# Performance work log

Hardware: AMD Instinct MI355X
Metric: run time of the kernel (lower is better)

## Reference

```python
import jax, jax.numpy as jnp
import numpy as np

B, S, E, H = 2, 2048, 1024, 16
DH = E // H


def setup_inputs() -> dict:
    key = jax.random.key(0)
    ks = jax.random.split(key, 9)
    inp = {
        "query": jax.random.normal(ks[0], (B, S, E), dtype=jnp.float32),
        "key": jax.random.normal(ks[1], (B, S, E), dtype=jnp.float32),
        "value": jax.random.normal(ks[2], (B, S, E), dtype=jnp.float32),
        # causal mask: True means "masked out" (masked_fill semantics)
        "mask": jnp.broadcast_to(
            jnp.triu(jnp.ones((S, S), dtype=bool), k=1)[None, None], (B, 1, S, S)
        ),
        # learned parameters (nn.Linear weight is [out, in]; y = x @ W.T + b)
        "Wq": jax.random.normal(ks[3], (E, E), dtype=jnp.float32) / np.sqrt(E),
        "Wk": jax.random.normal(ks[4], (E, E), dtype=jnp.float32) / np.sqrt(E),
        "Wv": jax.random.normal(ks[5], (E, E), dtype=jnp.float32) / np.sqrt(E),
        "Wo": jax.random.normal(ks[6], (E, E), dtype=jnp.float32) / np.sqrt(E),
        "bo": jax.random.normal(ks[7], (E,), dtype=jnp.float32) * 0.01,
    }
    return inp


def reference(query, key, value, mask, Wq, Wk, Wv, Wo, bo):
    # projections (no bias for q/k/v)
    Q = query @ Wq.T  # [B,S,E]
    K = key @ Wk.T
    V = value @ Wv.T
    # split heads: [B,S,E] -> [B,H,S,Dh]
    Q = Q.reshape(B, S, H, DH).transpose(0, 2, 1, 3)
    K = K.reshape(B, S, H, DH).transpose(0, 2, 1, 3)
    V = V.reshape(B, S, H, DH).transpose(0, 2, 1, 3)
    scale = 1.0 / np.sqrt(DH).astype(np.float32)
    scores = jnp.einsum("bhqd,bhkd->bhqk", Q, K) * scale  # [B,H,S,S]
    scores = jnp.where(mask, -jnp.inf, scores)
    attn = jax.nn.softmax(scores, axis=-1)
    # dropout(p=0.2) is identity in eval mode
    out = jnp.einsum("bhqk,bhkd->bhqd", attn, V)  # [B,H,S,Dh]
    out = out.transpose(0, 2, 1, 3).reshape(B, S, E)
    return out @ Wo.T + bo
```

## Files before the change

kernel.cpp:

```cpp
#include <hip/hip_runtime.h>
#include <hip/hip_bf16.h>
#include <stdint.h>

#define Bb 2
#define Ss 2048
#define Ee 1024
#define Hh 16
#define Dh 64

typedef __bf16 bf16_t;
typedef __attribute__((ext_vector_type(8))) __bf16 bf16x8;
typedef __attribute__((ext_vector_type(4))) __bf16 bf16x4;
typedef __attribute__((ext_vector_type(4))) float f32x4;

#define QSCALE_LOG2E 0.18033688011112042f

__device__ inline void gload_lds16(const void* g, void* l) {
  __builtin_amdgcn_global_load_lds((__attribute__((address_space(1))) void*)g,
                                   (__attribute__((address_space(3))) void*)l,
                                   16, 0, 0);
}

__device__ inline void wg_barrier() {
  asm volatile("s_barrier" ::: "memory");
}

__device__ __forceinline__ int p_addr(int q, int kv) {
  return q * 256 + ((((kv >> 3) ^ q) & 15) << 4) + (kv & 7) * 2;
}

struct Cvt7 {
  const float* s[7];
  bf16_t* d[7];
  int n8[7];
};

__global__ __launch_bounds__(256) void cvt_f32_bf16(Cvt7 c) {
  int gid = blockIdx.x * 256 + threadIdx.x;
#pragma unroll
  for (int j = 0; j < 7; ++j) {
    if (gid < c.n8[j]) {
      const float* s = c.s[j] + (size_t)gid * 8;
      const f32x4 lo = *(const f32x4*)s;
      const f32x4 hi = *(const f32x4*)(s + 4);
      bf16x8 v;
      v[0] = (bf16_t)lo[0]; v[1] = (bf16_t)lo[1];
      v[2] = (bf16_t)lo[2]; v[3] = (bf16_t)lo[3];
      v[4] = (bf16_t)hi[0]; v[5] = (bf16_t)hi[1];
      v[6] = (bf16_t)hi[2]; v[7] = (bf16_t)hi[3];
      *(bf16x8*)(c.d[j] + (size_t)gid * 8) = v;
      return;
    }
    gid -= c.n8[j];
  }
}

template <int ROWS>
__device__ __forceinline__ void stage_bf16(const bf16_t* __restrict__ src,
                                           int ldk, int k0, bf16_t* lds,
                                           int wave, int lane) {
  const int srow = lane >> 3, sslot = lane & 7;
#pragma unroll
  for (int r = 0; r < ROWS / 32; ++r) {
    const int chunk = wave + r * 4;
    const int row = chunk * 8 + srow;
    const int k16 = sslot ^ (row & 7);
    gload_lds16(src + (size_t)row * ldk + k0 + k16 * 8, lds + chunk * 512);
  }
}

template <typename EPI>
__device__ __forceinline__ void gemm_128x64(const bf16_t* Arow,
                                            const bf16_t* Wrow, bf16_t* As,
                                            bf16_t* Bs, int wave, int lane,
                                            EPI epi) {
  const int lr = lane & 15, lg = lane >> 4;
  f32x4 acc[2][4] = {};

  stage_bf16<128>(Arow, Ee, 0, As, wave, lane);
  stage_bf16<64>(Wrow, Ee, 0, Bs, wave, lane);
  stage_bf16<128>(Arow, Ee, 64, As + 8192, wave, lane);
  stage_bf16<64>(Wrow, Ee, 64, Bs + 4096, wave, lane);

  for (int t = 0; t < 16; ++t) {
    const int cur = t & 1;
    if (t < 15)
      asm volatile("s_waitcnt vmcnt(6)" ::: "memory");
    else
      asm volatile("s_waitcnt vmcnt(0)" ::: "memory");
    wg_barrier();

    const char* a_base = (const char*)(As + cur * 8192);
    const char* b_base = (const char*)(Bs + cur * 4096);
#pragma unroll
    for (int kk = 0; kk < 2; ++kk) {
      bf16x8 af[2], bfr[4];
#pragma unroll
      for (int x = 0; x < 2; ++x) {
        const int arow = wave * 32 + x * 16 + lr;
        af[x] = *(const bf16x8*)(a_base + ((arow * 128 + kk * 64 + lg * 16) ^
                                           ((arow & 7) << 4)));
      }
#pragma unroll
      for (int ni = 0; ni < 4; ++ni) {
        const int brow = ni * 16 + lr;
        bfr[ni] = *(const bf16x8*)(b_base + ((brow * 128 + kk * 64 + lg * 16) ^
                                             ((brow & 7) << 4)));
      }
#pragma unroll
      for (int mi = 0; mi < 2; ++mi)
#pragma unroll
        for (int ni = 0; ni < 4; ++ni)
          acc[mi][ni] = __builtin_amdgcn_mfma_f32_16x16x32_bf16(
              af[mi], bfr[ni], acc[mi][ni], 0, 0, 0);
    }
    wg_barrier();
    if (t + 2 < 16) {
      stage_bf16<128>(Arow, Ee, (t + 2) * 64, As + cur * 8192, wave, lane);
      stage_bf16<64>(Wrow, Ee, (t + 2) * 64, Bs + cur * 4096, wave, lane);
    }
  }

#pragma unroll
  for (int mi = 0; mi < 2; ++mi)
#pragma unroll
    for (int i = 0; i < 4; ++i) {
      const int mloc = wave * 32 + mi * 16 + lg * 4 + i;
#pragma unroll
      for (int ni = 0; ni < 4; ++ni)
        epi(mloc, ni * 16 + lr, acc[mi][ni][i]);
    }
}

__global__ __launch_bounds__(256) void qkv_proj(
    const bf16_t* __restrict__ Aq, const bf16_t* __restrict__ Ak,
    const bf16_t* __restrict__ Av, const bf16_t* __restrict__ Wq,
    const bf16_t* __restrict__ Wk, const bf16_t* __restrict__ Wv,
    bf16_t* __restrict__ Cq, bf16_t* __restrict__ Ck,
    bf16_t* __restrict__ Cv) {
  __shared__ bf16_t As[2][128 * 64];
  __shared__ bf16_t Bs[2][64 * 64];
  const int z = blockIdx.z;
  const bf16_t* A = (z == 0) ? Aq : (z == 1) ? Ak : Av;
  const bf16_t* W = (z == 0) ? Wq : (z == 1) ? Wk : Wv;
  bf16_t* C = (z == 0) ? Cq : (z == 1) ? Ck : Cv;

  const int wg = blockIdx.y * 16 + blockIdx.x;
  const int virt = (wg & 7) * 64 + (wg >> 3);
  const int n0 = (virt & 15) * 64, m0 = (virt >> 4) * 128;

  const int lane = threadIdx.x & 63, wave = threadIdx.x >> 6;

  gemm_128x64(A + (size_t)m0 * Ee, W + (size_t)n0 * Ee, As[0], Bs[0], wave,
              lane, [&](int mloc, int nloc, float v) {
                const int m = m0 + mloc, n = n0 + nloc;
                if (z == 0) v *= QSCALE_LOG2E;
                const int b = m >> 11, s = m & (Ss - 1);
                const int h = n >> 6, d = n & 63;
                if (z != 2)
                  C[(((size_t)(b * Hh + h)) * Ss + s) * Dh + d] = (bf16_t)v;
                else
                  C[(((size_t)(b * Hh + h)) * Dh + d) * Ss + s] = (bf16_t)v;
              });
}

__global__ __launch_bounds__(256) void out_gemm(const bf16_t* __restrict__ A,
                                                const bf16_t* __restrict__ W,
                                                const float* __restrict__ bias,
                                                float* __restrict__ C) {
  __shared__ bf16_t As[2][128 * 64];
  __shared__ bf16_t Bs[2][64 * 64];
  const int wg = blockIdx.y * 16 + blockIdx.x;
  const int virt = (wg & 7) * 64 + (wg >> 3);
  const int n0 = (virt & 15) * 64, m0 = (virt >> 4) * 128;

  const int lane = threadIdx.x & 63, wave = threadIdx.x >> 6;

  gemm_128x64(A + (size_t)m0 * Ee, W + (size_t)n0 * Ee, As[0], Bs[0], wave,
              lane, [&](int mloc, int nloc, float v) {
                const int n = n0 + nloc;
                C[(size_t)(m0 + mloc) * Ee + n] = v + bias[n];
              });
}


__device__ __forceinline__ void attn_stage(const bf16_t* Kh, const bf16_t* Vh,
                                           int kv0, int wave, int lane,
                                           bf16_t* KsBuf, bf16_t* VsBuf) {
#pragma unroll
  for (int r = 0; r < 8; ++r) {
    const int c = wave + r * 2;
    const int krow = c * 8 + (lane >> 3);
    const int ks = (lane & 7) ^ (krow & 7);
    gload_lds16(Kh + (size_t)(kv0 + krow) * Dh + ks * 8, KsBuf + c * 512);
    const int vrow = c * 4 + (lane >> 4);
    const int vs = (lane & 15) ^ (vrow & 7);
    gload_lds16(Vh + (size_t)vrow * Ss + kv0 + vs * 8, VsBuf + c * 512);
  }
}

template <int NI, bool MASKED>
__device__ __forceinline__ void attn_tile_compute(
    int kv0, int qw, int lane, char* pb, const char* kb, const char* vb,
    const bf16x8 aq[2][2], float m_run[2], float l_run[2], f32x4 oacc[2][4]) {
  const int lr = lane & 15, lg = lane >> 4;

  f32x4 sc[2][NI];
#pragma unroll
  for (int ni = 0; ni < NI; ++ni) {
    const int krow = ni * 16 + lr;
    const bf16x8 ak0 =
        *(const bf16x8*)(kb + ((krow * 128 + lg * 16) ^ ((krow & 7) << 4)));
    const bf16x8 ak1 = *(const bf16x8*)(kb + ((krow * 128 + 64 + lg * 16) ^
                                              ((krow & 7) << 4)));
#pragma unroll
    for (int qj = 0; qj < 2; ++qj) {
      f32x4 z = {0.f, 0.f, 0.f, 0.f};
      z = __builtin_amdgcn_mfma_f32_16x16x32_bf16(ak0, aq[qj][0], z, 0, 0, 0);
      z = __builtin_amdgcn_mfma_f32_16x16x32_bf16(ak1, aq[qj][1], z, 0, 0, 0);
      sc[qj][ni] = z;
    }
  }

  float corr[2];
#pragma unroll
  for (int qj = 0; qj < 2; ++qj) {
    if (MASKED) {
      const int q_rel = qw + qj * 16 + lr - kv0;
#pragma unroll
      for (int ni = 0; ni < NI; ++ni)
#pragma unroll
        for (int i = 0; i < 4; ++i)
          if (ni * 16 + lg * 4 + i > q_rel) sc[qj][ni][i] = -1e30f;
    }

    f32x4 vm = sc[qj][0];
#pragma unroll
    for (int ni = 1; ni < NI; ++ni)
#pragma unroll
      for (int i = 0; i < 4; ++i) vm[i] = fmaxf(vm[i], sc[qj][ni][i]);
    float rm = fmaxf(fmaxf(vm[0], vm[1]), fmaxf(vm[2], vm[3]));
    rm = fmaxf(rm, __shfl_xor(rm, 16));
    rm = fmaxf(rm, __shfl_xor(rm, 32));

    const float mo = m_run[qj];
    const float mn = fmaxf(mo, rm);
    corr[qj] = __builtin_amdgcn_exp2f(mo - mn);
    m_run[qj] = mn;

    f32x4 vs = {0.f, 0.f, 0.f, 0.f};
#pragma unroll
    for (int ni = 0; ni < NI; ++ni) {
      bf16x4 w;
#pragma unroll
      for (int i = 0; i < 4; ++i) {
        const float p = __builtin_amdgcn_exp2f(sc[qj][ni][i] - mn);
        vs[i] += p;
        w[i] = (bf16_t)p;
      }
      *(bf16x4*)(pb + p_addr(qj * 16 + lr, ni * 16 + lg * 4)) = w;
    }
    float rs = (vs[0] + vs[1]) + (vs[2] + vs[3]);
    rs += __shfl_xor(rs, 16);
    rs += __shfl_xor(rs, 32);
    l_run[qj] = l_run[qj] * corr[qj] + rs;

#pragma unroll
    for (int i = 0; i < 4; ++i) {
      const float ci = __shfl(corr[qj], (lane & 48) | (lg * 4 + i));
#pragma unroll
      for (int di = 0; di < 4; ++di) oacc[qj][di][i] *= ci;
    }
  }

#pragma unroll
  for (int kk = 0; kk < NI / 2; ++kk) {
    bf16x8 pa[2];
#pragma unroll
    for (int qj = 0; qj < 2; ++qj)
      pa[qj] =
          *(const bf16x8*)(pb + p_addr(qj * 16 + lr, kk * 32 + lg * 8));
#pragma unroll
    for (int di = 0; di < 4; ++di) {
      const int vrow = di * 16 + lr;
      const bf16x8 bv = *(const bf16x8*)(vb + ((vrow * 256 + kk * 64 +
                                                lg * 16) ^
                                               ((vrow & 7) << 4)));
#pragma unroll
      for (int qj = 0; qj < 2; ++qj)
        oacc[qj][di] = __builtin_amdgcn_mfma_f32_16x16x32_bf16(
            pa[qj], bv, oacc[qj][di], 0, 0, 0);
    }
  }
}

__device__ __forceinline__ void flash_qtile(int qt, const bf16_t* Qh,
                                            const bf16_t* Kh, const bf16_t* Vh,
                                            bf16_t* AO_row, int wave, int lane,
                                            bf16_t* Ks, bf16_t* Vs,
                                            bf16_t* PsW) {
  const int lr = lane & 15, lg = lane >> 4;
  const int qw = qt * 64 + wave * 32;

  bf16x8 aq[2][2];
#pragma unroll
  for (int qj = 0; qj < 2; ++qj)
#pragma unroll
    for (int kd = 0; kd < 2; ++kd)
      aq[qj][kd] = *(const bf16x8*)(Qh + (size_t)(qw + qj * 16 + lr) * Dh +
                                    kd * 32 + lg * 8);

  f32x4 oacc[2][4] = {};
  float m_run[2] = {-1e30f, -1e30f}, l_run[2] = {0.f, 0.f};
  char* pb = (char*)PsW;

  const int nt = (qt + 2) >> 1;
  attn_stage(Kh, Vh, 0, wave, lane, Ks, Vs);

  for (int t = 0; t < nt; ++t) {
    const int cur = t & 1;
    if (t + 1 < nt) {
      attn_stage(Kh, Vh, (t + 1) * 128, wave, lane, Ks + (cur ^ 1) * 8192,
                 Vs + (cur ^ 1) * 8192);
      asm volatile("s_waitcnt vmcnt(16)" ::: "memory");
    } else {
      asm volatile("s_waitcnt vmcnt(0)" ::: "memory");
    }
    wg_barrier();
    const char* kb = (const char*)(Ks + cur * 8192);
    const char* vb = (const char*)(Vs + cur * 8192);
    if (t < nt - 1)
      attn_tile_compute<8, false>(t * 128, qw, lane, pb, kb, vb, aq, m_run,
                                  l_run, oacc);
    else if ((qt & 1) == 0)
      attn_tile_compute<4, true>(t * 128, qw, lane, pb, kb, vb, aq, m_run,
                                 l_run, oacc);
    else
      attn_tile_compute<8, true>(t * 128, qw, lane, pb, kb, vb, aq, m_run,
                                 l_run, oacc);
    wg_barrier();
  }

#pragma unroll
  for (int qj = 0; qj < 2; ++qj) {
#pragma unroll
    for (int i = 0; i < 4; ++i) {
      const float li = __shfl(l_run[qj], (lane & 48) | (lg * 4 + i));
      const float inv = 1.0f / li;
      const int s = qw + qj * 16 + lg * 4 + i;
#pragma unroll
      for (int di = 0; di < 4; ++di) {
        const int d = di * 16 + lr;
        AO_row[(size_t)s * Ee + d] = (bf16_t)(oacc[qj][di][i] * inv);
      }
    }
  }
}

__global__ __launch_bounds__(128, 2) void attn_causal(
    const bf16_t* __restrict__ Qg, const bf16_t* __restrict__ Kg,
    const bf16_t* __restrict__ Vg, bf16_t* __restrict__ AO) {
  const int wg = blockIdx.y * 16 + blockIdx.x;
  const int virt = (wg & 7) * 64 + (wg >> 3);
  const int qx = virt & 15;
  const int bh = virt >> 4;

  const int tid = threadIdx.x;
  const int lane = tid & 63, wave = tid >> 6;

  const bf16_t* Qh = Qg + (size_t)bh * Ss * Dh;
  const bf16_t* Kh = Kg + (size_t)bh * Ss * Dh;
  const bf16_t* Vh = Vg + (size_t)bh * Dh * Ss;
  const int b = bh >> 4, h = bh & 15;
  bf16_t* AO_row = AO + (size_t)b * Ss * Ee + h * 64;

  __shared__ bf16_t Ks[2][128 * 64];
  __shared__ bf16_t Vs[2][64 * 128];
  __shared__ bf16_t Ps[2][32 * 128];

  const int qtA = qx;
  const int qtB = 31 - qx;
  flash_qtile(qtA, Qh, Kh, Vh, AO_row, wave, lane, Ks[0], Vs[0], Ps[wave]);
  flash_qtile(qtB, Qh, Kh, Vh, AO_row, wave, lane, Ks[0], Vs[0], Ps[wave]);
}

extern "C" void kernel_launch(void* const* d_in, const int* in_sizes, int n_in,
                              void* d_out, int out_size, void* d_ws,
                              size_t ws_size, hipStream_t stream) {
  const float* query = (const float*)d_in[0];
  const float* key = (const float*)d_in[1];
  const float* value = (const float*)d_in[2];
  const float* Wq = (const float*)d_in[4];
  const float* Wk = (const float*)d_in[5];
  const float* Wv = (const float*)d_in[6];
  const float* Wo = (const float*)d_in[7];
  const float* bo = (const float*)d_in[8];

  const size_t T = (size_t)Bb * Ss * Ee;
  const size_t WN = (size_t)Ee * Ee;
  bf16_t* qbf = (bf16_t*)d_ws;
  bf16_t* kbf = qbf + T;
  bf16_t* vbf = kbf + T;
  bf16_t* wqb = vbf + T;
  bf16_t* wkb = wqb + WN;
  bf16_t* wvb = wkb + WN;
  bf16_t* wob = wvb + WN;
  bf16_t* qws = wob + WN;
  bf16_t* kws = qws + T;
  bf16_t* vws = kws + T;
  bf16_t* aows = qbf;

  Cvt7 c;
  c.s[0] = query; c.d[0] = qbf; c.n8[0] = (int)(T / 8);
  c.s[1] = key;   c.d[1] = kbf; c.n8[1] = (int)(T / 8);
  c.s[2] = value; c.d[2] = vbf; c.n8[2] = (int)(T / 8);
  c.s[3] = Wq;    c.d[3] = wqb; c.n8[3] = (int)(WN / 8);
  c.s[4] = Wk;    c.d[4] = wkb; c.n8[4] = (int)(WN / 8);
  c.s[5] = Wv;    c.d[5] = wvb; c.n8[5] = (int)(WN / 8);
  c.s[6] = Wo;    c.d[6] = wob; c.n8[6] = (int)(WN / 8);
  const int total8 = (int)((3 * T + 4 * WN) / 8);

  dim3 blk(256);
  cvt_f32_bf16<<<dim3(total8 / 256), blk, 0, stream>>>(c);
  qkv_proj<<<dim3(Ee / 64, (Bb * Ss) / 128, 3), blk, 0, stream>>>(
      qbf, kbf, vbf, wqb, wkb, wvb, qws, kws, vws);
  attn_causal<<<dim3(16, Bb * Hh), dim3(128), 0, stream>>>(qws, kws, vws,
                                                           aows);
  out_gemm<<<dim3(Ee / 64, (Bb * Ss) / 128), blk, 0, stream>>>(
      aows, wob, bo, (float*)d_out);
}
```

Before: 124.1 us.

## Run both paired causal q-tiles concurrently with four waves sharing K/V tiles

Each attention workgroup now has four waves instead of two. The short q-tile and the long q-tile are processed at the same time, not one after the other, so the K/V tiles staged in shared memory are reused by both tiles and each wave issues fewer staging loads. Compute is split into 64-key halves so waves whose causal range ends sooner can skip work while the tile pipeline continues. The cost is a larger block, waves on the short tile sitting idle at barriers once their range is done, and a higher register and shared-memory footprint per block.

```diff
diff --git a/kernel.cpp b/kernel.cpp
--- a/kernel.cpp
+++ b/kernel.cpp
@@ -25,8 +25,8 @@
   asm volatile("s_barrier" ::: "memory");
 }
 
-__device__ __forceinline__ int p_addr(int q, int kv) {
-  return q * 256 + ((((kv >> 3) ^ q) & 15) << 4) + (kv & 7) * 2;
+__device__ __forceinline__ int p_addr32(int q, int kv) {
+  return q * 128 + ((((kv >> 3) ^ q) & 7) << 4) + (kv & 7) * 2;
 }
 
 struct Cvt7 {
@@ -188,8 +188,8 @@
                                            int kv0, int wave, int lane,
                                            bf16_t* KsBuf, bf16_t* VsBuf) {
 #pragma unroll
-  for (int r = 0; r < 8; ++r) {
-    const int c = wave + r * 2;
+  for (int r = 0; r < 4; ++r) {
+    const int c = wave + r * 4;
     const int krow = c * 8 + (lane >> 3);
     const int ks = (lane & 7) ^ (krow & 7);
     gload_lds16(Kh + (size_t)(kv0 + krow) * Dh + ks * 8, KsBuf + c * 512);
@@ -199,16 +199,19 @@
   }
 }
 
-template <int NI, bool MASKED>
-__device__ __forceinline__ void attn_tile_compute(
-    int kv0, int qw, int lane, char* pb, const char* kb, const char* vb,
-    const bf16x8 aq[2][2], float m_run[2], float l_run[2], f32x4 oacc[2][4]) {
+template <bool MASKED>
+__device__ __forceinline__ void attn_half(int kv0g, int hoff, int qw, int lane,
+                                          char* pb, const char* kb,
+                                          const char* vb,
+                                          const bf16x8 aq[2][2],
+                                          float m_run[2], float l_run[2],
+                                          f32x4 oacc[2][4]) {
   const int lr = lane & 15, lg = lane >> 4;
 
-  f32x4 sc[2][NI];
-#pragma unroll
-  for (int ni = 0; ni < NI; ++ni) {
-    const int krow = ni * 16 + lr;
+  f32x4 sc[2][4];
+#pragma unroll
+  for (int ni = 0; ni < 4; ++ni) {
+    const int krow = hoff * 64 + ni * 16 + lr;
     const bf16x8 ak0 =
         *(const bf16x8*)(kb + ((krow * 128 + lg * 16) ^ ((krow & 7) << 4)));
     const bf16x8 ak1 = *(const bf16x8*)(kb + ((krow * 128 + 64 + lg * 16) ^
@@ -222,13 +225,12 @@
     }
   }
 
-  float corr[2];
 #pragma unroll
   for (int qj = 0; qj < 2; ++qj) {
     if (MASKED) {
-      const int q_rel = qw + qj * 16 + lr - kv0;
-#pragma unroll
-      for (int ni = 0; ni < NI; ++ni)
+      const int q_rel = qw + qj * 16 + lr - kv0g;
+#pragma unroll
+      for (int ni = 0; ni < 4; ++ni)
 #pragma unroll
         for (int i = 0; i < 4; ++i)
           if (ni * 16 + lg * 4 + i > q_rel) sc[qj][ni][i] = -1e30f;
@@ -236,7 +238,7 @@
 
     f32x4 vm = sc[qj][0];
 #pragma unroll
-    for (int ni = 1; ni < NI; ++ni)
+    for (int ni = 1; ni < 4; ++ni)
 #pragma unroll
       for (int i = 0; i < 4; ++i) vm[i] = fmaxf(vm[i], sc[qj][ni][i]);
     float rm = fmaxf(fmaxf(vm[0], vm[1]), fmaxf(vm[2], vm[3]));
@@ -245,12 +247,12 @@
 
     const float mo = m_run[qj];
     const float mn = fmaxf(mo, rm);
-    corr[qj] = __builtin_amdgcn_exp2f(mo - mn);
+    const float corr = __builtin_amdgcn_exp2f(mo - mn);
     m_run[qj] = mn;
 
     f32x4 vs = {0.f, 0.f, 0.f, 0.f};
 #pragma unroll
-    for (int ni = 0; ni < NI; ++ni) {
+    for (int ni = 0; ni < 4; ++ni) {
       bf16x4 w;
 #pragma unroll
       for (int i = 0; i < 4; ++i) {
@@ -258,33 +260,32 @@
         vs[i] += p;
         w[i] = (bf16_t)p;
       }
-      *(bf16x4*)(pb + p_addr(qj * 16 + lr, ni * 16 + lg * 4)) = w;
+      *(bf16x4*)(pb + p_addr32(qj * 16 + lr, ni * 16 + lg * 4)) = w;
     }
     float rs = (vs[0] + vs[1]) + (vs[2] + vs[3]);
     rs += __shfl_xor(rs, 16);
     rs += __shfl_xor(rs, 32);
-    l_run[qj] = l_run[qj] * corr[qj] + rs;
+    l_run[qj] = l_run[qj] * corr + rs;
 
 #pragma unroll
     for (int i = 0; i < 4; ++i) {
-      const float ci = __shfl(corr[qj], (lane & 48) | (lg * 4 + i));
+      const float ci = __shfl(corr, (lane & 48) | (lg * 4 + i));
 #pragma unroll
       for (int di = 0; di < 4; ++di) oacc[qj][di][i] *= ci;
     }
   }
 
 #pragma unroll
-  for (int kk = 0; kk < NI / 2; ++kk) {
+  for (int kk = 0; kk < 2; ++kk) {
     bf16x8 pa[2];
 #pragma unroll
     for (int qj = 0; qj < 2; ++qj)
-      pa[qj] =
-          *(const bf16x8*)(pb + p_addr(qj * 16 + lr, kk * 32 + lg * 8));
+      pa[qj] = *(const bf16x8*)(pb + p_addr32(qj * 16 + lr, kk * 32 + lg * 8));
 #pragma unroll
     for (int di = 0; di < 4; ++di) {
       const int vrow = di * 16 + lr;
-      const bf16x8 bv = *(const bf16x8*)(vb + ((vrow * 256 + kk * 64 +
-                                                lg * 16) ^
+      const bf16x8 bv = *(const bf16x8*)(vb + ((vrow * 256 + hoff * 128 +
+                                                kk * 64 + lg * 16) ^
                                                ((vrow & 7) << 4)));
 #pragma unroll
       for (int qj = 0; qj < 2; ++qj)
@@ -294,70 +295,7 @@
   }
 }
 
-__device__ __forceinline__ void flash_qtile(int qt, const bf16_t* Qh,
-                                            const bf16_t* Kh, const bf16_t* Vh,
-                                            bf16_t* AO_row, int wave, int lane,
-                                            bf16_t* Ks, bf16_t* Vs,
-                                            bf16_t* PsW) {
-  const int lr = lane & 15, lg = lane >> 4;
-  const int qw = qt * 64 + wave * 32;
-
-  bf16x8 aq[2][2];
-#pragma unroll
-  for (int qj = 0; qj < 2; ++qj)
-#pragma unroll
-    for (int kd = 0; kd < 2; ++kd)
-      aq[qj][kd] = *(const bf16x8*)(Qh + (size_t)(qw + qj * 16 + lr) * Dh +
-                                    kd * 32 + lg * 8);
-
-  f32x4 oacc[2][4] = {};
-  float m_run[2] = {-1e30f, -1e30f}, l_run[2] = {0.f, 0.f};
-  char* pb = (char*)PsW;
-
-  const int nt = (qt + 2) >> 1;
-  attn_stage(Kh, Vh, 0, wave, lane, Ks, Vs);
-
-  for (int t = 0; t < nt; ++t) {
-    const int cur = t & 1;
-    if (t + 1 < nt) {
-      attn_stage(Kh, Vh, (t + 1) * 128, wave, lane, Ks + (cur ^ 1) * 8192,
-                 Vs + (cur ^ 1) * 8192);
-      asm volatile("s_waitcnt vmcnt(16)" ::: "memory");
-    } else {
-      asm volatile("s_waitcnt vmcnt(0)" ::: "memory");
-    }
-    wg_barrier();
-    const char* kb = (const char*)(Ks + cur * 8192);
-    const char* vb = (const char*)(Vs + cur * 8192);
-    if (t < nt - 1)
-      attn_tile_compute<8, false>(t * 128, qw, lane, pb, kb, vb, aq, m_run,
-                                  l_run, oacc);
-    else if ((qt & 1) == 0)
-      attn_tile_compute<4, true>(t * 128, qw, lane, pb, kb, vb, aq, m_run,
-                                 l_run, oacc);
-    else
-      attn_tile_compute<8, true>(t * 128, qw, lane, pb, kb, vb, aq, m_run,
-                                 l_run, oacc);
-    wg_barrier();
-  }
-
-#pragma unroll
-  for (int qj = 0; qj < 2; ++qj) {
-#pragma unroll
-    for (int i = 0; i < 4; ++i) {
-      const float li = __shfl(l_run[qj], (lane & 48) | (lg * 4 + i));
-      const float inv = 1.0f / li;
-      const int s = qw + qj * 16 + lg * 4 + i;
-#pragma unroll
-      for (int di = 0; di < 4; ++di) {
-        const int d = di * 16 + lr;
-        AO_row[(size_t)s * Ee + d] = (bf16_t)(oacc[qj][di][i] * inv);
-      }
-    }
-  }
-}
-
-__global__ __launch_bounds__(128, 2) void attn_causal(
+__global__ __launch_bounds__(256, 2) void attn_causal(
     const bf16_t* __restrict__ Qg, const bf16_t* __restrict__ Kg,
     const bf16_t* __restrict__ Vg, bf16_t* __restrict__ AO) {
   const int wg = blockIdx.y * 16 + blockIdx.x;
@@ -367,6 +305,7 @@
 
   const int tid = threadIdx.x;
   const int lane = tid & 63, wave = tid >> 6;
+  const int lr = lane & 15, lg = lane >> 4;
 
   const bf16_t* Qh = Qg + (size_t)bh * Ss * Dh;
   const bf16_t* Kh = Kg + (size_t)bh * Ss * Dh;
@@ -376,12 +315,68 @@
 
   __shared__ bf16_t Ks[2][128 * 64];
   __shared__ bf16_t Vs[2][64 * 128];
-  __shared__ bf16_t Ps[2][32 * 128];
-
-  const int qtA = qx;
-  const int qtB = 31 - qx;
-  flash_qtile(qtA, Qh, Kh, Vh, AO_row, wave, lane, Ks[0], Vs[0], Ps[wave]);
-  flash_qtile(qtB, Qh, Kh, Vh, AO_row, wave, lane, Ks[0], Vs[0], Ps[wave]);
+  __shared__ bf16_t Ps[4][32 * 64];
+
+  const int qt = (wave >> 1) ? (31 - qx) : qx;
+  const int qw = qt * 64 + (wave & 1) * 32;
+  const int nh = qt + 1;
+  const int ntB = (33 - qx) >> 1;
+
+  bf16x8 aq[2][2];
+#pragma unroll
+  for (int qj = 0; qj < 2; ++qj)
+#pragma unroll
+    for (int kd = 0; kd < 2; ++kd)
+      aq[qj][kd] = *(const bf16x8*)(Qh + (size_t)(qw + qj * 16 + lr) * Dh +
+                                    kd * 32 + lg * 8);
+
+  f32x4 oacc[2][4] = {};
+  float m_run[2] = {-1e30f, -1e30f}, l_run[2] = {0.f, 0.f};
+  char* pb = (char*)Ps[wave];
+
+  attn_stage(Kh, Vh, 0, wave, lane, Ks[0], Vs[0]);
+
+  for (int t = 0; t < ntB; ++t) {
+    const int cur = t & 1;
+    if (t + 1 < ntB) {
+      attn_stage(Kh, Vh, (t + 1) * 128, wave, lane, Ks[cur ^ 1], Vs[cur ^ 1]);
+      asm volatile("s_waitcnt vmcnt(8)" ::: "memory");
+    } else {
+      asm volatile("s_waitcnt vmcnt(0)" ::: "memory");
+    }
+    wg_barrier();
+    const char* kb = (const char*)Ks[cur];
+    const char* vb = (const char*)Vs[cur];
+
+#pragma unroll
+    for (int d = 0; d < 2; ++d) {
+      const int hh = 2 * t + d;
+      if (hh < nh) {
+        if (hh == nh - 1)
+          attn_half<true>(hh * 64, d, qw, lane, pb, kb, vb, aq, m_run, l_run,
+                          oacc);
+        else
+          attn_half<false>(hh * 64, d, qw, lane, pb, kb, vb, aq, m_run, l_run,
+                           oacc);
+      }
+    }
+    wg_barrier();
+  }
+
+#pragma unroll
+  for (int qj = 0; qj < 2; ++qj) {
+#pragma unroll
+    for (int i = 0; i < 4; ++i) {
+      const float li = __shfl(l_run[qj], (lane & 48) | (lg * 4 + i));
+      const float inv = 1.0f / li;
+      const int s = qw + qj * 16 + lg * 4 + i;
+#pragma unroll
+      for (int di = 0; di < 4; ++di) {
+        const int d = di * 16 + lr;
+        AO_row[(size_t)s * Ee + d] = (bf16_t)(oacc[qj][di][i] * inv);
+      }
+    }
+  }
 }
 
 extern "C" void kernel_launch(void* const* d_in, const int* in_sizes, int n_in,
@@ -424,8 +419,7 @@
   cvt_f32_bf16<<<dim3(total8 / 256), blk, 0, stream>>>(c);
   qkv_proj<<<dim3(Ee / 64, (Bb * Ss) / 128, 3), blk, 0, stream>>>(
       qbf, kbf, vbf, wqb, wkb, wvb, qws, kws, vws);
-  attn_causal<<<dim3(16, Bb * Hh), dim3(128), 0, stream>>>(qws, kws, vws,
-                                                           aows);
+  attn_causal<<<dim3(16, Bb * Hh), blk, 0, stream>>>(qws, kws, vws, aows);
   out_gemm<<<dim3(Ee / 64, (Bb * Ss) / 128), blk, 0, stream>>>(
       aows, wob, bo, (float*)d_out);
 }
```

Result: slower. 129.8 us (+4.6%).
